# Kernel tuning notes

Measured on AMD Instinct MI355X. Metric: run time of the kernel, lower is better.

## Reference

```python
import jax, jax.numpy as jnp
import numpy as np

B, D_IN = 4096, 1024
E, K = 16, 2
EMB = 256
H1, H2 = 2048, 1024  # hidden_units, hidden_units // 2
O = 512              # num_classes


def setup_inputs() -> dict:
    key = jax.random.key(0)
    ks = jax.random.split(key, 10)
    s = lambda *sh: 1.0 / np.sqrt(sh[-2] if len(sh) > 1 else 1.0)
    return {
        "x":   jax.random.normal(ks[0], (B, D_IN), jnp.float32),
        "Wr":  jax.random.normal(ks[1], (D_IN, EMB), jnp.float32) * (1.0 / np.sqrt(D_IN)),
        "br":  jnp.zeros((EMB,), jnp.float32),
        "emb": jax.random.normal(ks[2], (E, EMB), jnp.float32) * (1.0 / np.sqrt(EMB)),
        "W1":  jax.random.normal(ks[3], (E, D_IN, H1), jnp.float32) * (1.0 / np.sqrt(D_IN)),
        "b1":  jnp.zeros((E, H1), jnp.float32),
        "W2":  jax.random.normal(ks[4], (E, H1, H2), jnp.float32) * (1.0 / np.sqrt(H1)),
        "b2":  jnp.zeros((E, H2), jnp.float32),
        "W3":  jax.random.normal(ks[5], (E, H2, O), jnp.float32) * (1.0 / np.sqrt(H2)),
        "b3":  jnp.zeros((E, O), jnp.float32),
    }


def reference(x, Wr, br, emb, W1, b1, W2, b2, W3, b3):
    # Router query: [B, EMB]
    q = x @ Wr + br
    # Negative squared euclidean distance to expert embeddings -> scores [B, E]
    d2 = jnp.sum(jnp.square(q[:, None, :] - emb[None, :, :]), axis=-1)
    scores = -d2
    gating_probs = jax.nn.softmax(scores, axis=-1)  # [B, E]
    # Top-k selection + renormalized gates
    top_v, top_i = jax.lax.top_k(scores, K)          # [B, K]
    gates = jax.nn.softmax(top_v, axis=-1)           # [B, K]
    # All experts run on full batch (dense), batched over expert axis
    h1 = jax.nn.relu(jnp.einsum('bi,eih->beh', x, W1) + b1)   # [B, E, H1]
    h2 = jax.nn.relu(jnp.einsum('beh,ehm->bem', h1, W2) + b2)  # [B, E, H2]
    out = jnp.einsum('bem,emo->beo', h2, W3) + b3              # [B, E, O]
    # Gather top-k expert outputs per example and combine
    sel = jnp.take_along_axis(out, top_i[:, :, None], axis=1)  # [B, K, O]
    final = jnp.sum(sel * gates[:, :, None], axis=1)           # [B, O]
    return final, q, gating_probs
```

## Files before the change

kernel.cpp:

```cpp
#include <hip/hip_runtime.h>
#include <hip/hip_bf16.h>

using bf16 = __hip_bfloat16;
typedef __attribute__((ext_vector_type(8))) short bf16x8;
typedef __attribute__((ext_vector_type(8))) unsigned short u16x8;
typedef __attribute__((ext_vector_type(4))) float f32x4;

constexpr int BATCH = 4096;
constexpr int D_IN  = 1024;
constexpr int NEXP  = 16;
constexpr int EMB   = 256;
constexpr int H1    = 2048;
constexpr int H2    = 1024;
constexpr int OUTD  = 512;
constexpr int SLOTS = BATCH * 2;
constexpr int SLOTS_PAD = SLOTS + 256;
constexpr int MAX_T256 = SLOTS / 256 + NEXP;
constexpr int MAX_T128 = SLOTS / 128 + NEXP;
constexpr int K3    = 3 * D_IN;

constexpr size_t WS_XB     = 0;
constexpr size_t WS_XLO    = WS_XB     + (size_t)BATCH * D_IN * 2;
constexpr size_t WS_H1     = WS_XLO    + (size_t)BATCH * D_IN * 2;
constexpr size_t WS_H2     = WS_H1     + (size_t)SLOTS_PAD * H1 * 2;
constexpr size_t WS_OSL    = WS_H2     + (size_t)SLOTS_PAD * H2 * 2;
constexpr size_t WS_TOPI   = WS_OSL    + (size_t)SLOTS_PAD * OUTD * 4;
constexpr size_t WS_GATES  = WS_TOPI   + (size_t)SLOTS * 4;
constexpr size_t WS_SLOTOF = WS_GATES  + (size_t)SLOTS * 4;
constexpr size_t WS_TOKL   = WS_SLOTOF + (size_t)SLOTS * 4;
constexpr size_t WS_CNT    = WS_TOKL   + (size_t)SLOTS_PAD * 4;
constexpr size_t WS_TMAP256= WS_CNT    + 64 * 4;
constexpr size_t WS_TMAP128= WS_TMAP256+ (size_t)MAX_T256 * 8;
constexpr size_t WS_WR3    = ((WS_TMAP128 + (size_t)MAX_T128 * 8) + 255) & ~(size_t)255;
constexpr size_t WS_WT     = ((WS_WR3 + (size_t)EMB * K3 * 2) + 255) & ~(size_t)255;

__device__ __forceinline__ unsigned short f2bf(float f) {
    bf16 h = __float2bfloat16(f);
    return __builtin_bit_cast(unsigned short, h);
}
__device__ __forceinline__ float bf2f(unsigned short h) {
    return __builtin_bit_cast(float, (unsigned)h << 16);
}

__device__ __forceinline__ void gload16(const unsigned short* g, unsigned short* l) {
    __builtin_amdgcn_global_load_lds(
        (const __attribute__((address_space(1))) unsigned int*)g,
        (__attribute__((address_space(3))) unsigned int*)l, 16, 0, 0);
}

template <int N>
__device__ __forceinline__ void waitcnt_vm() {
    static_assert(N == 0 || N == 4 || N == 8, "add case");
    if constexpr (N == 0) asm volatile("s_waitcnt vmcnt(0)" ::: "memory");
    else if constexpr (N == 4) asm volatile("s_waitcnt vmcnt(4)" ::: "memory");
    else if constexpr (N == 8) asm volatile("s_waitcnt vmcnt(8)" ::: "memory");
}

__global__ __launch_bounds__(256) void k_cvt_x(const float* __restrict__ x,
                                               unsigned short* __restrict__ xhi,
                                               unsigned short* __restrict__ xlo) {
    int i = blockIdx.x * 256 + threadIdx.x;
    float4 v = reinterpret_cast<const float4*>(x)[i];
    ushort4 h, l;
    h.x = f2bf(v.x); h.y = f2bf(v.y); h.z = f2bf(v.z); h.w = f2bf(v.w);
    l.x = f2bf(v.x - bf2f(h.x)); l.y = f2bf(v.y - bf2f(h.y));
    l.z = f2bf(v.z - bf2f(h.z)); l.w = f2bf(v.w - bf2f(h.w));
    reinterpret_cast<ushort4*>(xhi)[i] = h;
    reinterpret_cast<ushort4*>(xlo)[i] = l;
}

__global__ __launch_bounds__(256) void k_wr3(const float* __restrict__ Wr,
                                             unsigned short* __restrict__ Wrt3) {
    __shared__ float Tf[64][65];
    int n0 = blockIdx.x * 64, k0 = blockIdx.y * 64;
    const float* Wb = Wr + (size_t)k0 * EMB + n0;
    int t  = threadIdx.x;
    int kr = t >> 4, c4 = (t & 15) * 4;
#pragma unroll
    for (int i = 0; i < 4; i++) {
        float4 v = *reinterpret_cast<const float4*>(Wb + (size_t)(kr + i * 16) * EMB + c4);
        Tf[kr + i * 16][c4 + 0] = v.x; Tf[kr + i * 16][c4 + 1] = v.y;
        Tf[kr + i * 16][c4 + 2] = v.z; Tf[kr + i * 16][c4 + 3] = v.w;
    }
    __syncthreads();
#pragma unroll
    for (int i = 0; i < 2; i++) {
        int idx = t + i * 256;
        int n = idx >> 3, ck = (idx & 7) * 8;
        u16x8 hi, lo;
#pragma unroll
        for (int j = 0; j < 8; j++) {
            float w = Tf[ck + j][n];
            unsigned short h = f2bf(w);
            hi[j] = h; lo[j] = f2bf(w - bf2f(h));
        }
        unsigned short* dst = Wrt3 + (size_t)(n0 + n) * K3 + k0 + ck;
        *reinterpret_cast<u16x8*>(dst)            = hi;
        *reinterpret_cast<u16x8*>(dst + D_IN)     = hi;
        *reinterpret_cast<u16x8*>(dst + 2 * D_IN) = lo;
    }
}

__global__ __launch_bounds__(256) void k_wtrans(const float* __restrict__ W,
                                                unsigned short* __restrict__ Wt,
                                                int KD, int ND) {
    __shared__ float Tf[64][65];
    int e = blockIdx.z;
    int n0 = blockIdx.x * 64, k0 = blockIdx.y * 64;
    const float* Wb = W + ((size_t)e * KD + k0) * ND + n0;
    int t  = threadIdx.x;
    int kr = t >> 4, c4 = (t & 15) * 4;
#pragma unroll
    for (int i = 0; i < 4; i++) {
        float4 v = *reinterpret_cast<const float4*>(Wb + (size_t)(kr + i * 16) * ND + c4);
        Tf[kr + i * 16][c4 + 0] = v.x; Tf[kr + i * 16][c4 + 1] = v.y;
        Tf[kr + i * 16][c4 + 2] = v.z; Tf[kr + i * 16][c4 + 3] = v.w;
    }
    __syncthreads();
    unsigned short* Wtb = Wt + ((size_t)e * ND + n0) * KD + k0;
#pragma unroll
    for (int i = 0; i < 2; i++) {
        int idx = t + i * 256;
        int n = idx >> 3, ck = (idx & 7) * 8;
        u16x8 o;
#pragma unroll
        for (int j = 0; j < 8; j++) o[j] = f2bf(Tf[ck + j][n]);
        *reinterpret_cast<u16x8*>(Wtb + (size_t)n * KD + ck) = o;
    }
}

__global__ __launch_bounds__(256) void k_router3(const unsigned short* __restrict__ xhi,
                                                 const unsigned short* __restrict__ xlo,
                                                 const unsigned short* __restrict__ wrt3,
                                                 const float* __restrict__ br,
                                                 float* __restrict__ qout) {
    int nb = blockIdx.x * 64;
    int mb = blockIdx.y * 64;

    __shared__ __align__(16) unsigned short As[2][64 * 64];
    __shared__ __align__(16) unsigned short Bs[2][64 * 64];

    int t    = threadIdx.x;
    int lane = t & 63;
    int w    = t >> 6;
    int wr   = (w >> 1) * 32;
    int wc   = (w & 1) * 32;

    int srow = t >> 3;
    int swz  = (t & 7) ^ (srow & 7);
    size_t aoff[2], boff[2];
#pragma unroll
    for (int i = 0; i < 2; i++) {
        int row = i * 32 + srow;
        aoff[i] = (size_t)(mb + row) * D_IN + swz * 8;
        boff[i] = (size_t)(nb + row) * K3 + swz * 8;
    }

    auto STAGE = [&](int buf, int tts) {
        const unsigned short* abase = (tts >= 16 && tts < 32) ? xlo : xhi;
        int kk = (tts & 15) * 64;
#pragma unroll
        for (int i = 0; i < 2; i++) {
            gload16(abase + aoff[i] + kk, &As[buf][(i * 32 + w * 8) * 64] + lane * 8);
            gload16(wrt3 + boff[i] + tts * 64, &Bs[buf][(i * 32 + w * 8) * 64] + lane * 8);
        }
    };

    f32x4 acc[2][2];
#pragma unroll
    for (int mi = 0; mi < 2; mi++)
#pragma unroll
        for (int ni = 0; ni < 2; ni++) acc[mi][ni] = {0.f, 0.f, 0.f, 0.f};

    int lr  = lane & 15;
    int lkc = lane >> 4;

    constexpr int NT = K3 / 64;
    STAGE(0, 0);
    STAGE(1, 1);

    for (int tt = 0; tt < NT; tt++) {
        int cur = tt & 1;
        if (tt + 1 < NT) waitcnt_vm<4>(); else waitcnt_vm<0>();
        __builtin_amdgcn_s_barrier();
        const char* Ab = (const char*)As[cur];
        const char* Bb = (const char*)Bs[cur];
#pragma unroll
        for (int ks = 0; ks < 2; ks++) {
            bf16x8 a[2], b[2];
#pragma unroll
            for (int mi = 0; mi < 2; mi++) {
                int row = wr + mi * 16 + lr;
                int c   = (lkc + ks * 4) ^ (row & 7);
                a[mi] = *reinterpret_cast<const bf16x8*>(Ab + row * 128 + c * 16);
            }
#pragma unroll
            for (int ni = 0; ni < 2; ni++) {
                int row = wc + ni * 16 + lr;
                int c   = (lkc + ks * 4) ^ (row & 7);
                b[ni] = *reinterpret_cast<const bf16x8*>(Bb + row * 128 + c * 16);
            }
#pragma unroll
            for (int mi = 0; mi < 2; mi++)
#pragma unroll
                for (int ni = 0; ni < 2; ni++)
                    acc[mi][ni] = __builtin_amdgcn_mfma_f32_16x16x32_bf16(a[mi], b[ni], acc[mi][ni], 0, 0, 0);
        }
        __builtin_amdgcn_s_barrier();
        if (tt + 2 < NT) STAGE(cur, tt + 2);
    }

    int rowbase = (lane >> 4) * 4;
#pragma unroll
    for (int ni = 0; ni < 2; ni++) {
        int col = nb + wc + ni * 16 + lr;
        float bv = br[col];
#pragma unroll
        for (int mi = 0; mi < 2; mi++) {
#pragma unroll
            for (int qi = 0; qi < 4; qi++) {
                int row = mb + wr + mi * 16 + rowbase + qi;
                qout[(size_t)row * EMB + col] = acc[mi][ni][qi] + bv;
            }
        }
    }
}

__global__ __launch_bounds__(256) void k_router_topk(const float* __restrict__ q,
                                                     const float* __restrict__ emb,
                                                     float* __restrict__ gp,
                                                     int* __restrict__ topi,
                                                     float* __restrict__ gates) {
    int b    = blockIdx.x * 4 + (threadIdx.x >> 6);
    int lane = threadIdx.x & 63;
    int e    = lane & 15;
    int seg  = (lane >> 4) * 64;
    const float* qr = q + (size_t)b * EMB + seg;
    const float* er = emb + (size_t)e * EMB + seg;
    float d2 = 0.f;
#pragma unroll 8
    for (int i = 0; i < 64; i++) { float d = qr[i] - er[i]; d2 = fmaf(d, d, d2); }
    d2 += __shfl_xor(d2, 16);
    d2 += __shfl_xor(d2, 32);
    float s = -d2;
    float m = s;
#pragma unroll
    for (int o = 1; o < 16; o <<= 1) m = fmaxf(m, __shfl_xor(m, o));
    float ex  = __expf(s - m);
    float sum = ex;
#pragma unroll
    for (int o = 1; o < 16; o <<= 1) sum += __shfl_xor(sum, o);
    if (lane < 16) gp[(size_t)b * NEXP + lane] = ex / sum;
    float v1 = s; int i1 = e;
#pragma unroll
    for (int o = 1; o < 16; o <<= 1) {
        float ov = __shfl_xor(v1, o); int oi = __shfl_xor(i1, o);
        if (ov > v1 || (ov == v1 && oi < i1)) { v1 = ov; i1 = oi; }
    }
    float s2 = (e == i1) ? -1e30f : s;
    float v2 = s2; int i2 = e;
#pragma unroll
    for (int o = 1; o < 16; o <<= 1) {
        float ov = __shfl_xor(v2, o); int oi = __shfl_xor(i2, o);
        if (ov > v2 || (ov == v2 && oi < i2)) { v2 = ov; i2 = oi; }
    }
    if (lane == 0) {
        topi[b * 2] = i1; topi[b * 2 + 1] = i2;
        float tv  = __expf(v2 - v1);
        float inv = 1.f / (1.f + tv);
        gates[b * 2] = inv; gates[b * 2 + 1] = tv * inv;
    }
}

__global__ void k_zero(int* counts) { if (threadIdx.x < NEXP) counts[threadIdx.x] = 0; }

__global__ __launch_bounds__(256) void k_count(const int* __restrict__ topi, int* __restrict__ counts) {
    int i = blockIdx.x * 256 + threadIdx.x;
    atomicAdd(&counts[topi[i]], 1);
}

__global__ void k_scan(const int* __restrict__ counts, int* __restrict__ offsets,
                       int* __restrict__ cursors, int2* __restrict__ tmap256,
                       int2* __restrict__ tmap128) {
    if (threadIdx.x != 0) return;
    int off = 0;
    for (int e = 0; e < NEXP; e++) {
        offsets[e] = off; cursors[e] = off;
        off += counts[e];
    }
    int n256 = 0, n128 = 0;
    for (int e = 0; e < NEXP; e++) {
        int c = counts[e];
        for (int base = 0; base < c; base += 256) tmap256[n256++] = make_int2(e, base);
        for (int base = 0; base < c; base += 128) tmap128[n128++] = make_int2(e, base);
    }
    for (; n256 < MAX_T256; n256++) tmap256[n256] = make_int2(-1, 0);
    for (; n128 < MAX_T128; n128++) tmap128[n128] = make_int2(-1, 0);
}

__global__ __launch_bounds__(256) void k_scatter(const int* __restrict__ topi, int* __restrict__ cursors,
                                                 int* __restrict__ toklist, int* __restrict__ slotof) {
    int i = blockIdx.x * 256 + threadIdx.x;
    int e = topi[i];
    int s = atomicAdd(&cursors[e], 1);
    toklist[s] = i >> 1;
    slotof[i]  = s;
}

template <int KD, int ND, int BM, int BN, int WM, int WN, int MODE, int MINW>
__global__ __launch_bounds__(WM * WN * 64, MINW) void k_gemm(
    const unsigned short* __restrict__ Xin, const unsigned short* __restrict__ Wt,
    const float* __restrict__ bg, unsigned short* __restrict__ Hout,
    float* __restrict__ Oout, const int* __restrict__ counts,
    const int* __restrict__ offsets, const int* __restrict__ toklist,
    const int2* __restrict__ tmap) {
    constexpr int THREADS = WM * WN * 64;
    constexpr int FM = BM / (WM * 16);
    constexpr int FN = BN / (WN * 16);
    constexpr int A_ISS = BM * 8 / THREADS;
    constexpr int B_ISS = BN * 8 / THREADS;
    constexpr int RPI = THREADS / 8;
    constexpr int SL  = A_ISS + B_ISS;

    int2 tm = tmap[blockIdx.y];
    int e = tm.x;
    if (e < 0) return;
    int base = tm.y;
    int n_e  = counts[e];
    int off  = offsets[e];
    int n0   = blockIdx.x * BN;

    __shared__ __align__(16) unsigned short As[2][BM * 64];
    __shared__ __align__(16) unsigned short Bs[2][BN * 64];

    int t    = threadIdx.x;
    int lane = t & 63;
    int w    = t >> 6;
    int wm   = w / WN;
    int wn   = w % WN;

    int srow  = t >> 3;
    int chunk = t & 7;
    const unsigned short* asrc[A_ISS];
    const unsigned short* bsrc[B_ISS];
#pragma unroll
    for (int i = 0; i < A_ISS; i++) {
        int row = i * RPI + srow;
        int swz = chunk ^ (row & 7);
        int g   = base + row;
        size_t arow;
        if (MODE == 0) {
            int gg = (g < n_e) ? g : (n_e - 1);
            arow = (size_t)toklist[off + gg];
        } else {
            arow = (size_t)(off + g);
        }
        asrc[i] = Xin + arow * KD + swz * 8;
    }
#pragma unroll
    for (int i = 0; i < B_ISS; i++) {
        int row = i * RPI + srow;
        int swz = chunk ^ (row & 7);
        bsrc[i] = Wt + ((size_t)e * ND + n0 + row) * KD + swz * 8;
    }

    auto STAGE = [&](int buf, int kt) {
#pragma unroll
        for (int i = 0; i < A_ISS; i++)
            gload16(asrc[i] + kt, &As[buf][(i * RPI + w * 8) * 64] + lane * 8);
#pragma unroll
        for (int i = 0; i < B_ISS; i++)
            gload16(bsrc[i] + kt, &Bs[buf][(i * RPI + w * 8) * 64] + lane * 8);
    };

    f32x4 acc[FM][FN];
#pragma unroll
    for (int mi = 0; mi < FM; mi++)
#pragma unroll
        for (int ni = 0; ni < FN; ni++) acc[mi][ni] = {0.f, 0.f, 0.f, 0.f};

    int lr  = lane & 15;
    int lkc = lane >> 4;

    constexpr int NT = KD / 64;
    STAGE(0, 0);
    STAGE(1, 64);

    for (int tt = 0; tt < NT; tt++) {
        int cur = tt & 1;
        if (tt + 1 < NT) waitcnt_vm<SL>(); else waitcnt_vm<0>();
        __builtin_amdgcn_s_barrier();
        const char* Ab = (const char*)As[cur];
        const char* Bb = (const char*)Bs[cur];
#pragma unroll
        for (int ks = 0; ks < 2; ks++) {
            bf16x8 b[FN];
#pragma unroll
            for (int ni = 0; ni < FN; ni++) {
                int row = wn * (BN / WN) + ni * 16 + lr;
                int c   = (lkc + ks * 4) ^ (row & 7);
                b[ni] = *reinterpret_cast<const bf16x8*>(Bb + row * 128 + c * 16);
            }
            bf16x8 a[FM];
#pragma unroll
            for (int mi = 0; mi < FM; mi++) {
                int row = wm * (BM / WM) + mi * 16 + lr;
                int c   = (lkc + ks * 4) ^ (row & 7);
                a[mi] = *reinterpret_cast<const bf16x8*>(Ab + row * 128 + c * 16);
            }
#pragma unroll
            for (int mi = 0; mi < FM; mi++)
#pragma unroll
                for (int ni = 0; ni < FN; ni++)
                    acc[mi][ni] = __builtin_amdgcn_mfma_f32_16x16x32_bf16(a[mi], b[ni], acc[mi][ni], 0, 0, 0);
        }
        __builtin_amdgcn_s_barrier();
        if (tt + 2 < NT) STAGE(cur, (tt + 2) * 64);
    }

    int rowbase = (lane >> 4) * 4;
#pragma unroll
    for (int ni = 0; ni < FN; ni++) {
        int col = n0 + wn * (BN / WN) + ni * 16 + lr;
        float bv = bg[(size_t)e * ND + col];
#pragma unroll
        for (int mi = 0; mi < FM; mi++) {
#pragma unroll
            for (int qi = 0; qi < 4; qi++) {
                int g = base + wm * (BM / WM) + mi * 16 + rowbase + qi;
                if (g < n_e) {
                    float v = acc[mi][ni][qi] + bv;
                    if (MODE == 2) {
                        Oout[(size_t)(off + g) * ND + col] = v;
                    } else {
                        v = fmaxf(v, 0.f);
                        Hout[(size_t)(off + g) * ND + col] = f2bf(v);
                    }
                }
            }
        }
    }
}

__global__ __launch_bounds__(128) void k_combine(const float* __restrict__ osl,
                                                 const float* __restrict__ gates,
                                                 const int* __restrict__ slotof,
                                                 float* __restrict__ outf) {
    int b = blockIdx.x;
    int j = threadIdx.x;
    int s0 = slotof[b * 2], s1 = slotof[b * 2 + 1];
    float g0 = gates[b * 2], g1 = gates[b * 2 + 1];
    float4 o0 = reinterpret_cast<const float4*>(osl + (size_t)s0 * OUTD)[j];
    float4 o1 = reinterpret_cast<const float4*>(osl + (size_t)s1 * OUTD)[j];
    float4 r;
    r.x = g0 * o0.x + g1 * o1.x;
    r.y = g0 * o0.y + g1 * o1.y;
    r.z = g0 * o0.z + g1 * o1.z;
    r.w = g0 * o0.w + g1 * o1.w;
    reinterpret_cast<float4*>(outf + (size_t)b * OUTD)[j] = r;
}

extern "C" void kernel_launch(void* const* d_in, const int* in_sizes, int n_in,
                              void* d_out, int out_size, void* d_ws, size_t ws_size,
                              hipStream_t stream) {
    const float* x   = (const float*)d_in[0];
    const float* Wr  = (const float*)d_in[1];
    const float* br  = (const float*)d_in[2];
    const float* emb = (const float*)d_in[3];
    const float* W1  = (const float*)d_in[4];
    const float* b1  = (const float*)d_in[5];
    const float* W2  = (const float*)d_in[6];
    const float* b2  = (const float*)d_in[7];
    const float* W3  = (const float*)d_in[8];
    const float* b3  = (const float*)d_in[9];

    float* out_final = (float*)d_out;
    float* out_q     = out_final + (size_t)BATCH * OUTD;
    float* out_gp    = out_q + (size_t)BATCH * EMB;

    char* ws = (char*)d_ws;
    unsigned short* xb  = (unsigned short*)(ws + WS_XB);
    unsigned short* xlo = (unsigned short*)(ws + WS_XLO);
    unsigned short* h1  = (unsigned short*)(ws + WS_H1);
    unsigned short* h2  = (unsigned short*)(ws + WS_H2);
    float* osl    = (float*)(ws + WS_OSL);
    int*   topi   = (int*)(ws + WS_TOPI);
    float* gates  = (float*)(ws + WS_GATES);
    int*   slotof = (int*)(ws + WS_SLOTOF);
    int*   toklist= (int*)(ws + WS_TOKL);
    int*   counts = (int*)(ws + WS_CNT);
    int*   offsets= counts + 16;
    int*   cursors= counts + 32;
    int2*  tmap256= (int2*)(ws + WS_TMAP256);
    int2*  tmap128= (int2*)(ws + WS_TMAP128);
    unsigned short* wrt3 = (unsigned short*)(ws + WS_WR3);
    unsigned short* wt   = (unsigned short*)(ws + WS_WT);

    k_cvt_x<<<BATCH * D_IN / 4 / 256, 256, 0, stream>>>(x, xb, xlo);
    k_wr3<<<dim3(EMB / 64, D_IN / 64), 256, 0, stream>>>(Wr, wrt3);
    k_router3<<<dim3(EMB / 64, BATCH / 64), 256, 0, stream>>>(xb, xlo, wrt3, br, out_q);
    k_router_topk<<<BATCH / 4, 256, 0, stream>>>(out_q, emb, out_gp, topi, gates);
    k_zero<<<1, 64, 0, stream>>>(counts);
    k_count<<<SLOTS / 256, 256, 0, stream>>>(topi, counts);
    k_scan<<<1, 64, 0, stream>>>(counts, offsets, cursors, tmap256, tmap128);
    k_scatter<<<SLOTS / 256, 256, 0, stream>>>(topi, cursors, toklist, slotof);

    k_wtrans<<<dim3(H1 / 64, D_IN / 64, NEXP), 256, 0, stream>>>(W1, wt, D_IN, H1);
    k_gemm<D_IN, H1, 256, 256, 2, 4, 0, 1><<<dim3(H1 / 256, MAX_T256), 512, 0, stream>>>(
        xb, wt, b1, h1, nullptr, counts, offsets, toklist, tmap256);

    k_wtrans<<<dim3(H2 / 64, H1 / 64, NEXP), 256, 0, stream>>>(W2, wt, H1, H2);
    k_gemm<H1, H2, 256, 256, 2, 4, 1, 1><<<dim3(H2 / 256, MAX_T256), 512, 0, stream>>>(
        h1, wt, b2, h2, nullptr, counts, offsets, toklist, tmap256);

    k_wtrans<<<dim3(OUTD / 64, H2 / 64, NEXP), 256, 0, stream>>>(W3, wt, H2, OUTD);
    k_gemm<H2, OUTD, 128, 128, 2, 2, 2, 2><<<dim3(OUTD / 128, MAX_T128), 256, 0, stream>>>(
        h2, wt, b3, nullptr, osl, counts, offsets, toklist, tmap128);

    k_combine<<<BATCH, 128, 0, stream>>>(osl, gates, slotof, out_final);
}
```

Before: 385.0 us.

## Split GEMM inner loop into barrier-synchronized phases with MFMA priority boost

For the two large expert GEMMs (256x256 tiles), each 64-wide K-step becomes four phases, each covering half the M fragments and one K sub-step. Each phase loads its fragments from LDS, waits on lgkmcnt, then issues MFMAs at raised wave priority, with block barriers and sched_barriers between phases. The aim is to keep waves in lockstep so LDS reads of some waves overlap the matrix math of others, and to lower register pressure by holding only half the A fragments at once. The cost is many more barriers per K-step, which can stall the pipeline. The last GEMM keeps the old path.

```diff
diff --git a/kernel.cpp b/kernel.cpp
--- a/kernel.cpp
+++ b/kernel.cpp
@@ -307,7 +307,7 @@
     slotof[i]  = s;
 }
 
-template <int KD, int ND, int BM, int BN, int WM, int WN, int MODE, int MINW>
+template <int KD, int ND, int BM, int BN, int WM, int WN, int MODE, int MINW, int PH>
 __global__ __launch_bounds__(WM * WN * 64, MINW) void k_gemm(
     const unsigned short* __restrict__ Xin, const unsigned short* __restrict__ Wt,
     const float* __restrict__ bg, unsigned short* __restrict__ Hout,
@@ -392,29 +392,65 @@
         __builtin_amdgcn_s_barrier();
         const char* Ab = (const char*)As[cur];
         const char* Bb = (const char*)Bs[cur];
-#pragma unroll
-        for (int ks = 0; ks < 2; ks++) {
-            bf16x8 b[FN];
-#pragma unroll
-            for (int ni = 0; ni < FN; ni++) {
-                int row = wn * (BN / WN) + ni * 16 + lr;
-                int c   = (lkc + ks * 4) ^ (row & 7);
-                b[ni] = *reinterpret_cast<const bf16x8*>(Bb + row * 128 + c * 16);
+
+        if constexpr (PH == 1) {
+            constexpr int FMH = FM / 2;
+#pragma unroll
+            for (int p = 0; p < 4; p++) {
+                const int mq = p >> 1;
+                const int ks = p & 1;
+                bf16x8 a[FMH], b[FN];
+#pragma unroll
+                for (int mi = 0; mi < FMH; mi++) {
+                    int row = wm * (BM / WM) + (mq * FMH + mi) * 16 + lr;
+                    int c   = (lkc + ks * 4) ^ (row & 7);
+                    a[mi] = *reinterpret_cast<const bf16x8*>(Ab + row * 128 + c * 16);
+                }
+#pragma unroll
+                for (int ni = 0; ni < FN; ni++) {
+                    int row = wn * (BN / WN) + ni * 16 + lr;
+                    int c   = (lkc + ks * 4) ^ (row & 7);
+                    b[ni] = *reinterpret_cast<const bf16x8*>(Bb + row * 128 + c * 16);
+                }
+                __builtin_amdgcn_s_barrier();
+                asm volatile("s_waitcnt lgkmcnt(0)" ::: "memory");
+                __builtin_amdgcn_sched_barrier(0);
+                __builtin_amdgcn_s_setprio(1);
+#pragma unroll
+                for (int mi = 0; mi < FMH; mi++)
+#pragma unroll
+                    for (int ni = 0; ni < FN; ni++)
+                        acc[mq * FMH + mi][ni] = __builtin_amdgcn_mfma_f32_16x16x32_bf16(
+                            a[mi], b[ni], acc[mq * FMH + mi][ni], 0, 0, 0);
+                __builtin_amdgcn_s_setprio(0);
+                __builtin_amdgcn_sched_barrier(0);
+                __builtin_amdgcn_s_barrier();
             }
-            bf16x8 a[FM];
-#pragma unroll
-            for (int mi = 0; mi < FM; mi++) {
-                int row = wm * (BM / WM) + mi * 16 + lr;
-                int c   = (lkc + ks * 4) ^ (row & 7);
-                a[mi] = *reinterpret_cast<const bf16x8*>(Ab + row * 128 + c * 16);
+        } else {
+#pragma unroll
+            for (int ks = 0; ks < 2; ks++) {
+                bf16x8 b[FN];
+#pragma unroll
+                for (int ni = 0; ni < FN; ni++) {
+                    int row = wn * (BN / WN) + ni * 16 + lr;
+                    int c   = (lkc + ks * 4) ^ (row & 7);
+                    b[ni] = *reinterpret_cast<const bf16x8*>(Bb + row * 128 + c * 16);
+                }
+                bf16x8 a[FM];
+#pragma unroll
+                for (int mi = 0; mi < FM; mi++) {
+                    int row = wm * (BM / WM) + mi * 16 + lr;
+                    int c   = (lkc + ks * 4) ^ (row & 7);
+                    a[mi] = *reinterpret_cast<const bf16x8*>(Ab + row * 128 + c * 16);
+                }
+#pragma unroll
+                for (int mi = 0; mi < FM; mi++)
+#pragma unroll
+                    for (int ni = 0; ni < FN; ni++)
+                        acc[mi][ni] = __builtin_amdgcn_mfma_f32_16x16x32_bf16(a[mi], b[ni], acc[mi][ni], 0, 0, 0);
             }
-#pragma unroll
-            for (int mi = 0; mi < FM; mi++)
-#pragma unroll
-                for (int ni = 0; ni < FN; ni++)
-                    acc[mi][ni] = __builtin_amdgcn_mfma_f32_16x16x32_bf16(a[mi], b[ni], acc[mi][ni], 0, 0, 0);
-        }
-        __builtin_amdgcn_s_barrier();
+            __builtin_amdgcn_s_barrier();
+        }
         if (tt + 2 < NT) STAGE(cur, (tt + 2) * 64);
     }
 
@@ -506,15 +542,15 @@
     k_scatter<<<SLOTS / 256, 256, 0, stream>>>(topi, cursors, toklist, slotof);
 
     k_wtrans<<<dim3(H1 / 64, D_IN / 64, NEXP), 256, 0, stream>>>(W1, wt, D_IN, H1);
-    k_gemm<D_IN, H1, 256, 256, 2, 4, 0, 1><<<dim3(H1 / 256, MAX_T256), 512, 0, stream>>>(
+    k_gemm<D_IN, H1, 256, 256, 2, 4, 0, 1, 1><<<dim3(H1 / 256, MAX_T256), 512, 0, stream>>>(
         xb, wt, b1, h1, nullptr, counts, offsets, toklist, tmap256);
 
     k_wtrans<<<dim3(H2 / 64, H1 / 64, NEXP), 256, 0, stream>>>(W2, wt, H1, H2);
-    k_gemm<H1, H2, 256, 256, 2, 4, 1, 1><<<dim3(H2 / 256, MAX_T256), 512, 0, stream>>>(
+    k_gemm<H1, H2, 256, 256, 2, 4, 1, 1, 1><<<dim3(H2 / 256, MAX_T256), 512, 0, stream>>>(
         h1, wt, b2, h2, nullptr, counts, offsets, toklist, tmap256);
 
     k_wtrans<<<dim3(OUTD / 64, H2 / 64, NEXP), 256, 0, stream>>>(W3, wt, H2, OUTD);
-    k_gemm<H2, OUTD, 128, 128, 2, 2, 2, 2><<<dim3(OUTD / 128, MAX_T128), 256, 0, stream>>>(
+    k_gemm<H2, OUTD, 128, 128, 2, 2, 2, 2, 0><<<dim3(OUTD / 128, MAX_T128), 256, 0, stream>>>(
         h2, wt, b3, nullptr, osl, counts, offsets, toklist, tmap128);
 
     k_combine<<<BATCH, 128, 0, stream>>>(osl, gates, slotof, out_final);
```

Result: slower. 421.5 us (+9.5%).

## Restructure grouped expert GEMM to 128x256 tiles with K=32 triple-buffered LDS pipeline

Applied to the files above, without the earlier changes.

Rewrites the grouped MoE GEMM kernel to use 4 waves each owning a 128x64 sub-tile (BM=128, BN=256), a K-step of 32 with a new LDS swizzle that packs two rows per 128-byte line, and a three-stage LDS ring buffer with deeper vmcnt waits. All three expert GEMMs now share a single 128-row tile map, which reduces padding waste from uneven expert counts and lets two blocks share each CU. The trade-off is fewer MFMAs per barrier (K=32 steps double the barrier count) and higher per-thread accumulator register pressure (32 accumulator fragments per thread).

```diff
diff --git a/kernel.cpp b/kernel.cpp
--- a/kernel.cpp
+++ b/kernel.cpp
@@ -15,7 +15,6 @@
 constexpr int OUTD  = 512;
 constexpr int SLOTS = BATCH * 2;
 constexpr int SLOTS_PAD = SLOTS + 256;
-constexpr int MAX_T256 = SLOTS / 256 + NEXP;
 constexpr int MAX_T128 = SLOTS / 128 + NEXP;
 constexpr int K3    = 3 * D_IN;
 
@@ -29,9 +28,8 @@
 constexpr size_t WS_SLOTOF = WS_GATES  + (size_t)SLOTS * 4;
 constexpr size_t WS_TOKL   = WS_SLOTOF + (size_t)SLOTS * 4;
 constexpr size_t WS_CNT    = WS_TOKL   + (size_t)SLOTS_PAD * 4;
-constexpr size_t WS_TMAP256= WS_CNT    + 64 * 4;
-constexpr size_t WS_TMAP128= WS_TMAP256+ (size_t)MAX_T256 * 8;
-constexpr size_t WS_WR3    = ((WS_TMAP128 + (size_t)MAX_T128 * 8) + 255) & ~(size_t)255;
+constexpr size_t WS_TMAP   = WS_CNT    + 64 * 4;
+constexpr size_t WS_WR3    = ((WS_TMAP + (size_t)MAX_T128 * 8) + 255) & ~(size_t)255;
 constexpr size_t WS_WT     = ((WS_WR3 + (size_t)EMB * K3 * 2) + 255) & ~(size_t)255;
 
 __device__ __forceinline__ unsigned short f2bf(float f) {
@@ -50,10 +48,13 @@
 
 template <int N>
 __device__ __forceinline__ void waitcnt_vm() {
-    static_assert(N == 0 || N == 4 || N == 8, "add case");
-    if constexpr (N == 0) asm volatile("s_waitcnt vmcnt(0)" ::: "memory");
-    else if constexpr (N == 4) asm volatile("s_waitcnt vmcnt(4)" ::: "memory");
-    else if constexpr (N == 8) asm volatile("s_waitcnt vmcnt(8)" ::: "memory");
+    if constexpr (N == 0)       asm volatile("s_waitcnt vmcnt(0)" ::: "memory");
+    else if constexpr (N == 4)  asm volatile("s_waitcnt vmcnt(4)" ::: "memory");
+    else if constexpr (N == 6)  asm volatile("s_waitcnt vmcnt(6)" ::: "memory");
+    else if constexpr (N == 8)  asm volatile("s_waitcnt vmcnt(8)" ::: "memory");
+    else if constexpr (N == 12) asm volatile("s_waitcnt vmcnt(12)" ::: "memory");
+    else if constexpr (N == 16) asm volatile("s_waitcnt vmcnt(16)" ::: "memory");
+    else static_assert(N == 0, "add case");
 }
 
 __global__ __launch_bounds__(256) void k_cvt_x(const float* __restrict__ x,
@@ -280,22 +281,19 @@
 }
 
 __global__ void k_scan(const int* __restrict__ counts, int* __restrict__ offsets,
-                       int* __restrict__ cursors, int2* __restrict__ tmap256,
-                       int2* __restrict__ tmap128) {
+                       int* __restrict__ cursors, int2* __restrict__ tmap) {
     if (threadIdx.x != 0) return;
     int off = 0;
     for (int e = 0; e < NEXP; e++) {
         offsets[e] = off; cursors[e] = off;
         off += counts[e];
     }
-    int n256 = 0, n128 = 0;
+    int nt = 0;
     for (int e = 0; e < NEXP; e++) {
         int c = counts[e];
-        for (int base = 0; base < c; base += 256) tmap256[n256++] = make_int2(e, base);
-        for (int base = 0; base < c; base += 128) tmap128[n128++] = make_int2(e, base);
-    }
-    for (; n256 < MAX_T256; n256++) tmap256[n256] = make_int2(-1, 0);
-    for (; n128 < MAX_T128; n128++) tmap128[n128] = make_int2(-1, 0);
+        for (int base = 0; base < c; base += 128) tmap[nt++] = make_int2(e, base);
+    }
+    for (; nt < MAX_T128; nt++) tmap[nt] = make_int2(-1, 0);
 }
 
 __global__ __launch_bounds__(256) void k_scatter(const int* __restrict__ topi, int* __restrict__ cursors,
@@ -307,20 +305,22 @@
     slotof[i]  = s;
 }
 
-template <int KD, int ND, int BM, int BN, int WM, int WN, int MODE, int MINW>
-__global__ __launch_bounds__(WM * WN * 64, MINW) void k_gemm(
+template <int KD, int ND, int WN, int MODE>
+__global__ __launch_bounds__(WN * 64, 2) void k_gemm(
     const unsigned short* __restrict__ Xin, const unsigned short* __restrict__ Wt,
     const float* __restrict__ bg, unsigned short* __restrict__ Hout,
     float* __restrict__ Oout, const int* __restrict__ counts,
     const int* __restrict__ offsets, const int* __restrict__ toklist,
     const int2* __restrict__ tmap) {
-    constexpr int THREADS = WM * WN * 64;
-    constexpr int FM = BM / (WM * 16);
-    constexpr int FN = BN / (WN * 16);
-    constexpr int A_ISS = BM * 8 / THREADS;
-    constexpr int B_ISS = BN * 8 / THREADS;
-    constexpr int RPI = THREADS / 8;
-    constexpr int SL  = A_ISS + B_ISS;
+    constexpr int THREADS = WN * 64;
+    constexpr int BM = 128;
+    constexpr int BN = WN * 64;
+    constexpr int FM = 8;
+    constexpr int FN = 4;
+    constexpr int RPI   = THREADS / 8;
+    constexpr int A_ISS = (BM / 2) / RPI;
+    constexpr int B_ISS = (BN / 2) / RPI;
+    constexpr int SL    = A_ISS + B_ISS;
 
     int2 tm = tmap[blockIdx.y];
     int e = tm.x;
@@ -330,14 +330,13 @@
     int off  = offsets[e];
     int n0   = blockIdx.x * BN;
 
-    __shared__ __align__(16) unsigned short As[2][BM * 64];
-    __shared__ __align__(16) unsigned short Bs[2][BN * 64];
+    __shared__ __align__(16) unsigned short As[3][(BM / 2) * 64];
+    __shared__ __align__(16) unsigned short Bs[3][(BN / 2) * 64];
 
     int t    = threadIdx.x;
     int lane = t & 63;
     int w    = t >> 6;
-    int wm   = w / WN;
-    int wn   = w % WN;
+    int wn   = w;
 
     int srow  = t >> 3;
     int chunk = t & 7;
@@ -345,9 +344,11 @@
     const unsigned short* bsrc[B_ISS];
 #pragma unroll
     for (int i = 0; i < A_ISS; i++) {
-        int row = i * RPI + srow;
-        int swz = chunk ^ (row & 7);
-        int g   = base + row;
+        int r  = i * RPI + srow;
+        int js = chunk ^ (r & 7);
+        int m_local = 2 * r + (js >> 2);
+        int koff    = (js & 3) * 8;
+        int g = base + m_local;
         size_t arow;
         if (MODE == 0) {
             int gg = (g < n_e) ? g : (n_e - 1);
@@ -355,13 +356,15 @@
         } else {
             arow = (size_t)(off + g);
         }
-        asrc[i] = Xin + arow * KD + swz * 8;
+        asrc[i] = Xin + arow * KD + koff;
     }
 #pragma unroll
     for (int i = 0; i < B_ISS; i++) {
-        int row = i * RPI + srow;
-        int swz = chunk ^ (row & 7);
-        bsrc[i] = Wt + ((size_t)e * ND + n0 + row) * KD + swz * 8;
+        int r  = i * RPI + srow;
+        int js = chunk ^ (r & 7);
+        int n_local = 2 * r + (js >> 2);
+        int koff    = (js & 3) * 8;
+        bsrc[i] = Wt + ((size_t)e * ND + n0 + n_local) * KD + koff;
     }
 
     auto STAGE = [&](int buf, int kt) {
@@ -381,53 +384,50 @@
 
     int lr  = lane & 15;
     int lkc = lane >> 4;
-
-    constexpr int NT = KD / 64;
+    int jrd    = (((lr & 1) << 2) + lkc) ^ ((lr >> 1) & 7);
+    int abase_ = (lr >> 1) * 128 + jrd * 16;
+    int bbase_ = wn * 4096 + (lr >> 1) * 128 + jrd * 16;
+
+    constexpr int NT = KD / 32;
     STAGE(0, 0);
-    STAGE(1, 64);
-
+    STAGE(1, 32);
+    STAGE(2, 64);
+
+    int cur = 0;
     for (int tt = 0; tt < NT; tt++) {
-        int cur = tt & 1;
-        if (tt + 1 < NT) waitcnt_vm<SL>(); else waitcnt_vm<0>();
+        if (tt + 2 < NT)      waitcnt_vm<2 * SL>();
+        else if (tt + 1 < NT) waitcnt_vm<SL>();
+        else                  waitcnt_vm<0>();
         __builtin_amdgcn_s_barrier();
         const char* Ab = (const char*)As[cur];
         const char* Bb = (const char*)Bs[cur];
-#pragma unroll
-        for (int ks = 0; ks < 2; ks++) {
-            bf16x8 b[FN];
-#pragma unroll
-            for (int ni = 0; ni < FN; ni++) {
-                int row = wn * (BN / WN) + ni * 16 + lr;
-                int c   = (lkc + ks * 4) ^ (row & 7);
-                b[ni] = *reinterpret_cast<const bf16x8*>(Bb + row * 128 + c * 16);
-            }
-            bf16x8 a[FM];
-#pragma unroll
-            for (int mi = 0; mi < FM; mi++) {
-                int row = wm * (BM / WM) + mi * 16 + lr;
-                int c   = (lkc + ks * 4) ^ (row & 7);
-                a[mi] = *reinterpret_cast<const bf16x8*>(Ab + row * 128 + c * 16);
-            }
-#pragma unroll
-            for (int mi = 0; mi < FM; mi++)
-#pragma unroll
-                for (int ni = 0; ni < FN; ni++)
-                    acc[mi][ni] = __builtin_amdgcn_mfma_f32_16x16x32_bf16(a[mi], b[ni], acc[mi][ni], 0, 0, 0);
-        }
+        bf16x8 a[FM], b[FN];
+#pragma unroll
+        for (int ni = 0; ni < FN; ni++)
+            b[ni] = *reinterpret_cast<const bf16x8*>(Bb + bbase_ + ni * 1024);
+#pragma unroll
+        for (int mi = 0; mi < FM; mi++)
+            a[mi] = *reinterpret_cast<const bf16x8*>(Ab + abase_ + mi * 1024);
+#pragma unroll
+        for (int mi = 0; mi < FM; mi++)
+#pragma unroll
+            for (int ni = 0; ni < FN; ni++)
+                acc[mi][ni] = __builtin_amdgcn_mfma_f32_16x16x32_bf16(a[mi], b[ni], acc[mi][ni], 0, 0, 0);
         __builtin_amdgcn_s_barrier();
-        if (tt + 2 < NT) STAGE(cur, (tt + 2) * 64);
+        if (tt + 3 < NT) STAGE(cur, (tt + 3) * 32);
+        cur = (cur == 2) ? 0 : cur + 1;
     }
 
     int rowbase = (lane >> 4) * 4;
 #pragma unroll
     for (int ni = 0; ni < FN; ni++) {
-        int col = n0 + wn * (BN / WN) + ni * 16 + lr;
+        int col = n0 + wn * 64 + ni * 16 + lr;
         float bv = bg[(size_t)e * ND + col];
 #pragma unroll
         for (int mi = 0; mi < FM; mi++) {
 #pragma unroll
             for (int qi = 0; qi < 4; qi++) {
-                int g = base + wm * (BM / WM) + mi * 16 + rowbase + qi;
+                int g = base + mi * 16 + rowbase + qi;
                 if (g < n_e) {
                     float v = acc[mi][ni][qi] + bv;
                     if (MODE == 2) {
@@ -491,8 +491,7 @@
     int*   counts = (int*)(ws + WS_CNT);
     int*   offsets= counts + 16;
     int*   cursors= counts + 32;
-    int2*  tmap256= (int2*)(ws + WS_TMAP256);
-    int2*  tmap128= (int2*)(ws + WS_TMAP128);
+    int2*  tmap   = (int2*)(ws + WS_TMAP);
     unsigned short* wrt3 = (unsigned short*)(ws + WS_WR3);
     unsigned short* wt   = (unsigned short*)(ws + WS_WT);
 
@@ -502,20 +501,20 @@
     k_router_topk<<<BATCH / 4, 256, 0, stream>>>(out_q, emb, out_gp, topi, gates);
     k_zero<<<1, 64, 0, stream>>>(counts);
     k_count<<<SLOTS / 256, 256, 0, stream>>>(topi, counts);
-    k_scan<<<1, 64, 0, stream>>>(counts, offsets, cursors, tmap256, tmap128);
+    k_scan<<<1, 64, 0, stream>>>(counts, offsets, cursors, tmap);
     k_scatter<<<SLOTS / 256, 256, 0, stream>>>(topi, cursors, toklist, slotof);
 
     k_wtrans<<<dim3(H1 / 64, D_IN / 64, NEXP), 256, 0, stream>>>(W1, wt, D_IN, H1);
-    k_gemm<D_IN, H1, 256, 256, 2, 4, 0, 1><<<dim3(H1 / 256, MAX_T256), 512, 0, stream>>>(
-        xb, wt, b1, h1, nullptr, counts, offsets, toklist, tmap256);
+    k_gemm<D_IN, H1, 4, 0><<<dim3(H1 / 256, MAX_T128), 256, 0, stream>>>(
+        xb, wt, b1, h1, nullptr, counts, offsets, toklist, tmap);
 
     k_wtrans<<<dim3(H2 / 64, H1 / 64, NEXP), 256, 0, stream>>>(W2, wt, H1, H2);
-    k_gemm<H1, H2, 256, 256, 2, 4, 1, 1><<<dim3(H2 / 256, MAX_T256), 512, 0, stream>>>(
-        h1, wt, b2, h2, nullptr, counts, offsets, toklist, tmap256);
+    k_gemm<H1, H2, 4, 1><<<dim3(H2 / 256, MAX_T128), 256, 0, stream>>>(
+        h1, wt, b2, h2, nullptr, counts, offsets, toklist, tmap);
 
     k_wtrans<<<dim3(OUTD / 64, H2 / 64, NEXP), 256, 0, stream>>>(W3, wt, H2, OUTD);
-    k_gemm<H2, OUTD, 128, 128, 2, 2, 2, 2><<<dim3(OUTD / 128, MAX_T128), 256, 0, stream>>>(
-        h2, wt, b3, nullptr, osl, counts, offsets, toklist, tmap128);
+    k_gemm<H2, OUTD, 4, 2><<<dim3(OUTD / 256, MAX_T128), 256, 0, stream>>>(
+        h2, wt, b3, nullptr, osl, counts, offsets, toklist, tmap);
 
     k_combine<<<BATCH, 128, 0, stream>>>(osl, gates, slotof, out_final);
 }
```

Measured after the change: 400.9 us. 4.1% more time.

## Bin-pack expert tiles into XCD-aligned bins for grouped GEMM scheduling

Applied to the files above, without the earlier changes.

The scan kernel now assigns expert row-tiles into 8 bins of fixed capacity, placing each tile in the least-loaded bin. The GEMM grid becomes 1D, and blockIdx modulo 8 selects the bin, which matches the round-robin dispatch of workgroups across the 8 XCDs. This aims to balance work per XCD and to keep tiles of the same expert (and so the same weights) on one XCD for L2 reuse. If the total tile count exceeds 8*CAP (48 or 80), tiles are silently dropped, so the result is only correct while the per-bin capacity is never exceeded.

```diff
diff --git a/kernel.cpp b/kernel.cpp
--- a/kernel.cpp
+++ b/kernel.cpp
@@ -288,14 +288,42 @@
         offsets[e] = off; cursors[e] = off;
         off += counts[e];
     }
-    int n256 = 0, n128 = 0;
-    for (int e = 0; e < NEXP; e++) {
-        int c = counts[e];
-        for (int base = 0; base < c; base += 256) tmap256[n256++] = make_int2(e, base);
-        for (int base = 0; base < c; base += 128) tmap128[n128++] = make_int2(e, base);
-    }
-    for (; n256 < MAX_T256; n256++) tmap256[n256] = make_int2(-1, 0);
-    for (; n128 < MAX_T128; n128++) tmap128[n128] = make_int2(-1, 0);
+    for (int i = 0; i < MAX_T256; i++) tmap256[i] = make_int2(-1, 0);
+    for (int i = 0; i < MAX_T128; i++) tmap128[i] = make_int2(-1, 0);
+    {
+        int binload[8] = {0, 0, 0, 0, 0, 0, 0, 0};
+        for (int e = 0; e < NEXP; e++) {
+            int rem = (counts[e] + 255) >> 8, ti = 0;
+            while (rem > 0) {
+                int b = 0;
+                for (int q2 = 1; q2 < 8; q2++)
+                    if (binload[q2] < binload[b]) b = q2;
+                int space = 6 - binload[b];
+                if (space <= 0) break;
+                int take = (rem < space) ? rem : space;
+                for (int i = 0; i < take; i++)
+                    tmap256[b * 6 + binload[b] + i] = make_int2(e, (ti + i) * 256);
+                binload[b] += take; ti += take; rem -= take;
+            }
+        }
+    }
+    {
+        int binload[8] = {0, 0, 0, 0, 0, 0, 0, 0};
+        for (int e = 0; e < NEXP; e++) {
+            int rem = (counts[e] + 127) >> 7, ti = 0;
+            while (rem > 0) {
+                int b = 0;
+                for (int q2 = 1; q2 < 8; q2++)
+                    if (binload[q2] < binload[b]) b = q2;
+                int space = 10 - binload[b];
+                if (space <= 0) break;
+                int take = (rem < space) ? rem : space;
+                for (int i = 0; i < take; i++)
+                    tmap128[b * 10 + binload[b] + i] = make_int2(e, (ti + i) * 128);
+                binload[b] += take; ti += take; rem -= take;
+            }
+        }
+    }
 }
 
 __global__ __launch_bounds__(256) void k_scatter(const int* __restrict__ topi, int* __restrict__ cursors,
@@ -307,7 +335,7 @@
     slotof[i]  = s;
 }
 
-template <int KD, int ND, int BM, int BN, int WM, int WN, int MODE, int MINW>
+template <int KD, int ND, int BM, int BN, int WM, int WN, int MODE, int MINW, int CAP>
 __global__ __launch_bounds__(WM * WN * 64, MINW) void k_gemm(
     const unsigned short* __restrict__ Xin, const unsigned short* __restrict__ Wt,
     const float* __restrict__ bg, unsigned short* __restrict__ Hout,
@@ -322,13 +350,19 @@
     constexpr int RPI = THREADS / 8;
     constexpr int SL  = A_ISS + B_ISS;
 
-    int2 tm = tmap[blockIdx.y];
+    int id  = blockIdx.x;
+    int bin = id & 7;
+    int j   = id >> 3;
+    int y   = bin * CAP + j % CAP;
+    int xnb = j / CAP;
+
+    int2 tm = tmap[y];
     int e = tm.x;
     if (e < 0) return;
     int base = tm.y;
     int n_e  = counts[e];
     int off  = offsets[e];
-    int n0   = blockIdx.x * BN;
+    int n0   = xnb * BN;
 
     __shared__ __align__(16) unsigned short As[2][BM * 64];
     __shared__ __align__(16) unsigned short Bs[2][BN * 64];
@@ -506,15 +540,15 @@
     k_scatter<<<SLOTS / 256, 256, 0, stream>>>(topi, cursors, toklist, slotof);
 
     k_wtrans<<<dim3(H1 / 64, D_IN / 64, NEXP), 256, 0, stream>>>(W1, wt, D_IN, H1);
-    k_gemm<D_IN, H1, 256, 256, 2, 4, 0, 1><<<dim3(H1 / 256, MAX_T256), 512, 0, stream>>>(
+    k_gemm<D_IN, H1, 256, 256, 2, 4, 0, 1, 6><<<(H1 / 256) * 48, 512, 0, stream>>>(
         xb, wt, b1, h1, nullptr, counts, offsets, toklist, tmap256);
 
     k_wtrans<<<dim3(H2 / 64, H1 / 64, NEXP), 256, 0, stream>>>(W2, wt, H1, H2);
-    k_gemm<H1, H2, 256, 256, 2, 4, 1, 1><<<dim3(H2 / 256, MAX_T256), 512, 0, stream>>>(
+    k_gemm<H1, H2, 256, 256, 2, 4, 1, 1, 6><<<(H2 / 256) * 48, 512, 0, stream>>>(
         h1, wt, b2, h2, nullptr, counts, offsets, toklist, tmap256);
 
     k_wtrans<<<dim3(OUTD / 64, H2 / 64, NEXP), 256, 0, stream>>>(W3, wt, H2, OUTD);
-    k_gemm<H2, OUTD, 128, 128, 2, 2, 2, 2><<<dim3(OUTD / 128, MAX_T128), 256, 0, stream>>>(
+    k_gemm<H2, OUTD, 128, 128, 2, 2, 2, 2, 10><<<(OUTD / 128) * 80, 256, 0, stream>>>(
         h2, wt, b3, nullptr, osl, counts, offsets, toklist, tmap128);
 
     k_combine<<<BATCH, 128, 0, stream>>>(osl, gates, slotof, out_final);
```

After: 385.4 us. About the same (+0.1%).
